# Kernel tuning notes

Hardware: AMD Instinct MI355X
Metric: run time of the kernel (lower is better)

Reference implementation:

```python
import jax, jax.numpy as jnp
import numpy as np

B, OUT, IN = 1024, 1024, 512


def setup_inputs() -> dict:
    key = jax.random.key(0)
    kx, kw = jax.random.split(key)
    X = jax.random.normal(kx, (B, IN), dtype=jnp.float32)
    # Xavier-uniform init for W [out_features, in_features]
    limit = float(np.sqrt(6.0 / (IN + OUT)))
    W = jax.random.uniform(kw, (OUT, IN), dtype=jnp.float32, minval=-limit, maxval=limit)
    return {"X": X, "W": W}


def reference(X, W):
    # tropical min-plus + max-plus 'matmul':
    # out[b,o] = min_i(W[o,i] + X[b,i]) + max_i(W[o,i] + X[b,i])
    S = X[:, None, :] + W[None, :, :]  # [B, OUT, IN]
    return jnp.min(S, axis=-1) + jnp.max(S, axis=-1)  # [B, OUT]
```

## Files before the change

### kernel.cpp

```cpp
#include <hip/hip_runtime.h>
#include <math.h>


typedef float f4 __attribute__((ext_vector_type(4)));

constexpr int B_DIM  = 1024;
constexpr int O_DIM  = 1024;
constexpr int IN_DIM = 512;

constexpr int NB = 64;
constexpr int NO = 16;
constexpr int KW = 64;

__global__ __launch_bounds__(512) void tropical_gemm(
    const float* __restrict__ X, const float* __restrict__ W,
    float* __restrict__ out) {
    __shared__ float lds[8192];

    const int tid  = threadIdx.x;
    const int w    = tid >> 6;
    const int lane = tid & 63;
    const int b0   = blockIdx.y * NB;
    const int o0   = blockIdx.x * NO;
    const int wu   = __builtin_amdgcn_readfirstlane(w);

    f4 xq[16];
    {
        const float* xp = X + (size_t)(b0 + lane) * IN_DIM + wu * KW;
#pragma unroll
        for (int j = 0; j < 16; ++j) xq[j] = *(const f4*)(xp + 4 * j);
    }

    const float* wbase = W + (size_t)o0 * IN_DIM + wu * KW;

    float mn[NO], mx[NO];
#pragma unroll
    for (int o = 0; o < NO; ++o) { mn[o] = INFINITY; mx[o] = -INFINITY; }

#pragma unroll
    for (int o = 0; o < NO; ++o) {
        const float* wr = wbase + (size_t)o * IN_DIM;
#pragma unroll
        for (int k = 0; k < KW; k += 2) {
            float s0 = xq[k >> 2][k & 3] + wr[k];
            float s1 = xq[(k + 1) >> 2][(k + 1) & 3] + wr[k + 1];
            asm("v_min3_f32 %0, %1, %2, %0"
                : "+v"(mn[o]) : "v"(s0), "v"(s1));
            asm("v_max3_f32 %0, %1, %2, %0"
                : "+v"(mx[o]) : "v"(s0), "v"(s1));
        }
    }

#define DUMP_STATE(slot)                                                      \
    do {                                                                      \
        float* p_ = lds + (slot) * 2048 + lane * 4;                           \
        _Pragma("unroll")                                                     \
        for (int c_ = 0; c_ < 4; ++c_) {                                      \
            f4 vn_ = {mn[4 * c_], mn[4 * c_ + 1], mn[4 * c_ + 2], mn[4 * c_ + 3]}; \
            f4 vx_ = {mx[4 * c_], mx[4 * c_ + 1], mx[4 * c_ + 2], mx[4 * c_ + 3]}; \
            *(f4*)(p_ + c_ * 256)       = vn_;                                \
            *(f4*)(p_ + (4 + c_) * 256) = vx_;                                \
        }                                                                     \
    } while (0)

#define MERGE_STATE(slot)                                                     \
    do {                                                                      \
        const float* p_ = lds + (slot) * 2048 + lane * 4;                     \
        _Pragma("unroll")                                                     \
        for (int c_ = 0; c_ < 4; ++c_) {                                      \
            f4 vn_ = *(const f4*)(p_ + c_ * 256);                             \
            f4 vx_ = *(const f4*)(p_ + (4 + c_) * 256);                       \
            mn[4 * c_]     = fminf(mn[4 * c_],     vn_[0]);                   \
            mn[4 * c_ + 1] = fminf(mn[4 * c_ + 1], vn_[1]);                   \
            mn[4 * c_ + 2] = fminf(mn[4 * c_ + 2], vn_[2]);                   \
            mn[4 * c_ + 3] = fminf(mn[4 * c_ + 3], vn_[3]);                   \
            mx[4 * c_]     = fmaxf(mx[4 * c_],     vx_[0]);                   \
            mx[4 * c_ + 1] = fmaxf(mx[4 * c_ + 1], vx_[1]);                   \
            mx[4 * c_ + 2] = fmaxf(mx[4 * c_ + 2], vx_[2]);                   \
            mx[4 * c_ + 3] = fmaxf(mx[4 * c_ + 3], vx_[3]);                   \
        }                                                                     \
    } while (0)

    __syncthreads();
    if (w >= 4) DUMP_STATE(w - 4);
    __syncthreads();
    if (w < 4) MERGE_STATE(w);
    __syncthreads();
    if (w == 2) DUMP_STATE(0);
    if (w == 3) DUMP_STATE(1);
    __syncthreads();
    if (w == 0) MERGE_STATE(0);
    if (w == 1) MERGE_STATE(1);
    __syncthreads();
    if (w == 1) DUMP_STATE(0);
    __syncthreads();
    if (w == 0) {
        MERGE_STATE(0);
        float* op = out + (size_t)(b0 + lane) * O_DIM + o0;
#pragma unroll
        for (int c = 0; c < 4; ++c) {
            f4 v = {mn[4 * c]     + mx[4 * c],
                    mn[4 * c + 1] + mx[4 * c + 1],
                    mn[4 * c + 2] + mx[4 * c + 2],
                    mn[4 * c + 3] + mx[4 * c + 3]};
            *(f4*)(op + 4 * c) = v;
        }
    }
#undef DUMP_STATE
#undef MERGE_STATE
}

extern "C" void kernel_launch(void* const* d_in, const int* in_sizes, int n_in,
                              void* d_out, int out_size, void* d_ws, size_t ws_size,
                              hipStream_t stream) {
    (void)in_sizes; (void)n_in; (void)d_ws; (void)ws_size; (void)out_size;
    const float* X = (const float*)d_in[0];
    const float* W = (const float*)d_in[1];
    float* out     = (float*)d_out;

    dim3 grid(O_DIM / NO, B_DIM / NB);
    tropical_gemm<<<grid, dim3(512), 0, stream>>>(X, W, out);
}
```

Baseline: 37.49 us.

## Stage W and X tiles through LDS with padded rows and software-pipelined W reads

The W tile for the block is copied into LDS once, and X rows are staged through a padded LDS buffer so each wave gets its 64-column slice via coalesced global loads instead of strided per-lane loads. The inner loop now reads W from LDS as f4 vectors, with four registers prefetched ahead of use, instead of issuing scalar global/constant loads per element. Launch bounds add a minimum occupancy hint. This trades extra LDS usage and eight barriers during X staging for fewer uncoalesced global accesses.

```diff
diff --git a/kernel.cpp b/kernel.cpp
--- a/kernel.cpp
+++ b/kernel.cpp
@@ -12,48 +12,99 @@
 constexpr int NO = 16;
 constexpr int KW = 64;
 
-__global__ __launch_bounds__(512) void tropical_gemm(
+constexpr int XREG     = 64 * 68;
+constexpr int WREG_OFF = XREG;
+
+__global__ __launch_bounds__(512, 4) void tropical_gemm(
     const float* __restrict__ X, const float* __restrict__ W,
     float* __restrict__ out) {
-    __shared__ float lds[8192];
+    __shared__ float lds[XREG + 16 * 512];
 
     const int tid  = threadIdx.x;
     const int w    = tid >> 6;
     const int lane = tid & 63;
     const int b0   = blockIdx.y * NB;
     const int o0   = blockIdx.x * NO;
-    const int wu   = __builtin_amdgcn_readfirstlane(w);
+
+    {
+        const int o   = tid >> 5;
+        const int kq0 = tid & 31;
+        const float* wp = W + (size_t)(o0 + o) * IN_DIM;
+        float* dst = lds + WREG_OFF + o * 512;
+#pragma unroll
+        for (int p = 0; p < 4; ++p) {
+            const int kq = kq0 + p * 32;
+            *(f4*)(dst + kq * 4) = *(const f4*)(wp + kq * 4);
+        }
+    }
 
     f4 xq[16];
     {
-        const float* xp = X + (size_t)(b0 + lane) * IN_DIM + wu * KW;
+        const int r  = tid >> 3;
+        const int q0 = tid & 7;
+        const float* xrow = X + (size_t)(b0 + r) * IN_DIM;
+        f4 ga = *(const f4*)(xrow + q0 * 4);
+        f4 gb = *(const f4*)(xrow + (q0 + 8) * 4);
+        for (int c = 0; c < 8; ++c) {
+            *(f4*)(lds + r * 68 + q0 * 4)       = ga;
+            *(f4*)(lds + r * 68 + (q0 + 8) * 4) = gb;
+            __syncthreads();
+            if (c < 7) {
+                ga = *(const f4*)(xrow + (c + 1) * 64 + q0 * 4);
+                gb = *(const f4*)(xrow + (c + 1) * 64 + (q0 + 8) * 4);
+            }
+            if (w == c) {
 #pragma unroll
-        for (int j = 0; j < 16; ++j) xq[j] = *(const f4*)(xp + 4 * j);
+                for (int j = 0; j < 16; ++j)
+                    xq[j] = *(const f4*)(lds + lane * 68 + j * 4);
+            }
+            __syncthreads();
+        }
     }
-
-    const float* wbase = W + (size_t)o0 * IN_DIM + wu * KW;
 
     float mn[NO], mx[NO];
 #pragma unroll
     for (int o = 0; o < NO; ++o) { mn[o] = INFINITY; mx[o] = -INFINITY; }
 
+    const char* wb = (const char*)(lds + WREG_OFF) + w * 256;
+
+#define LOADW(P, Q)                                                           \
+    P = *(const f4*)(wb + ((Q) >> 4) * 2048 + ((Q) & 15) * 16)
+
+#define CMPQ(P, Q)                                                            \
+    do {                                                                      \
+        float s0_ = xq[(Q) & 15][0] + P[0];                                   \
+        float s1_ = xq[(Q) & 15][1] + P[1];                                   \
+        float s2_ = xq[(Q) & 15][2] + P[2];                                   \
+        float s3_ = xq[(Q) & 15][3] + P[3];                                   \
+        asm("v_min3_f32 %0, %1, %2, %0"                                       \
+            : "+v"(mn[(Q) >> 4]) : "v"(s0_), "v"(s1_));                       \
+        asm("v_max3_f32 %0, %1, %2, %0"                                       \
+            : "+v"(mx[(Q) >> 4]) : "v"(s0_), "v"(s1_));                       \
+        asm("v_min3_f32 %0, %1, %2, %0"                                       \
+            : "+v"(mn[(Q) >> 4]) : "v"(s2_), "v"(s3_));                       \
+        asm("v_max3_f32 %0, %1, %2, %0"                                       \
+            : "+v"(mx[(Q) >> 4]) : "v"(s2_), "v"(s3_));                       \
+    } while (0)
+
+    {
+        f4 wA, wB, wC, wD;
+        LOADW(wA, 0); LOADW(wB, 1); LOADW(wC, 2); LOADW(wD, 3);
 #pragma unroll
-    for (int o = 0; o < NO; ++o) {
-        const float* wr = wbase + (size_t)o * IN_DIM;
-#pragma unroll
-        for (int k = 0; k < KW; k += 2) {
-            float s0 = xq[k >> 2][k & 3] + wr[k];
-            float s1 = xq[(k + 1) >> 2][(k + 1) & 3] + wr[k + 1];
-            asm("v_min3_f32 %0, %1, %2, %0"
-                : "+v"(mn[o]) : "v"(s0), "v"(s1));
-            asm("v_max3_f32 %0, %1, %2, %0"
-                : "+v"(mx[o]) : "v"(s0), "v"(s1));
+        for (int qp = 0; qp < 63; ++qp) {
+            CMPQ(wA, 4 * qp);     LOADW(wA, 4 * qp + 4);
+            CMPQ(wB, 4 * qp + 1); LOADW(wB, 4 * qp + 5);
+            CMPQ(wC, 4 * qp + 2); LOADW(wC, 4 * qp + 6);
+            CMPQ(wD, 4 * qp + 3); LOADW(wD, 4 * qp + 7);
         }
+        CMPQ(wA, 252); CMPQ(wB, 253); CMPQ(wC, 254); CMPQ(wD, 255);
     }
+#undef LOADW
+#undef CMPQ
 
 #define DUMP_STATE(slot)                                                      \
     do {                                                                      \
-        float* p_ = lds + (slot) * 2048 + lane * 4;                           \
+        float* p_ = lds + WREG_OFF + (slot) * 2048 + lane * 4;                \
         _Pragma("unroll")                                                     \
         for (int c_ = 0; c_ < 4; ++c_) {                                      \
             f4 vn_ = {mn[4 * c_], mn[4 * c_ + 1], mn[4 * c_ + 2], mn[4 * c_ + 3]}; \
@@ -65,7 +116,7 @@
 
 #define MERGE_STATE(slot)                                                     \
     do {                                                                      \
-        const float* p_ = lds + (slot) * 2048 + lane * 4;                     \
+        const float* p_ = lds + WREG_OFF + (slot) * 2048 + lane * 4;          \
         _Pragma("unroll")                                                     \
         for (int c_ = 0; c_ < 4; ++c_) {                                      \
             f4 vn_ = *(const f4*)(p_ + c_ * 256);                             \
```

After: 35.75 us. 4.6% less time.

## Use 64x64 register-tiled tropical GEMM with LDS staging and split-K combine

Applied to the files above, without the earlier changes.

Replaces the per-warp 64x16 layout, which re-read W rows from global memory, with a 64x64 output tile per block. Each lane now holds an 8x8 register micro-tile of min/max accumulators, and X/W are staged through double-buffered LDS. The K dimension is split across 4 waves plus optionally 2 blocks in z, with a separate combine kernel that reduces the partial min/max results from the workspace. This raises arithmetic intensity per load, at the cost of 128 accumulator registers, an extra kernel launch, and extra global traffic through the workspace.

```diff
diff --git a/kernel.cpp b/kernel.cpp
--- a/kernel.cpp
+++ b/kernel.cpp
@@ -3,88 +3,168 @@
 
 
 typedef float f4 __attribute__((ext_vector_type(4)));
+typedef float f2 __attribute__((ext_vector_type(2)));
 
 constexpr int B_DIM  = 1024;
 constexpr int O_DIM  = 1024;
 constexpr int IN_DIM = 512;
-
-constexpr int NB = 64;
-constexpr int NO = 16;
-constexpr int KW = 64;
-
-__global__ __launch_bounds__(512) void tropical_gemm(
+constexpr int TILE   = 64;
+constexpr int P      = B_DIM * O_DIM;
+
+template <int KSPLIT>
+__global__ __launch_bounds__(256) void tropical_gemm(
     const float* __restrict__ X, const float* __restrict__ W,
-    float* __restrict__ out) {
-    __shared__ float lds[8192];
+    float* __restrict__ out, float* __restrict__ ws) {
+    constexpr int KW     = (KSPLIT == 2) ? 64 : 128;
+    constexpr int NSTAGE = KW / 8;
+    __shared__ float lds[16384];
 
     const int tid  = threadIdx.x;
     const int w    = tid >> 6;
     const int lane = tid & 63;
-    const int b0   = blockIdx.y * NB;
-    const int o0   = blockIdx.x * NO;
-    const int wu   = __builtin_amdgcn_readfirstlane(w);
-
-    f4 xq[16];
-    {
-        const float* xp = X + (size_t)(b0 + lane) * IN_DIM + wu * KW;
-#pragma unroll
-        for (int j = 0; j < 16; ++j) xq[j] = *(const f4*)(xp + 4 * j);
+    const int im   = lane >> 3;
+    const int in_  = lane & 7;
+    const int b0   = blockIdx.y * TILE;
+    const int o0   = blockIdx.x * TILE;
+    const int kh   = (KSPLIT == 2) ? blockIdx.z : 0;
+    const int kbase = kh * (IN_DIM / KSPLIT) + w * KW;
+
+    const float* Xp = X + (size_t)(b0 + lane) * IN_DIM + kbase;
+    const float* Wp = W + (size_t)(o0 + lane) * IN_DIM + kbase;
+
+    float* wbase = &lds[w * 2048];
+    const int stw = ((lane & 7) >> 1) * 32 + (lane >> 3) * 4 + (lane & 1) * 2;
+
+    float mn[8][8], mx[8][8];
+#pragma unroll
+    for (int i = 0; i < 8; ++i)
+#pragma unroll
+        for (int j = 0; j < 8; ++j) { mn[i][j] = INFINITY; mx[i][j] = -INFINITY; }
+
+#define PF(S)                                                                 \
+    do {                                                                      \
+        xa = *(const f4*)(Xp + (S) * 8);                                      \
+        xb = *(const f4*)(Xp + (S) * 8 + 4);                                  \
+        wa = *(const f4*)(Wp + (S) * 8);                                      \
+        wb = *(const f4*)(Wp + (S) * 8 + 4);                                  \
+    } while (0)
+
+#define STAGE(BUF)                                                            \
+    do {                                                                      \
+        float* dX_ = wbase + (BUF) * 1024;                                    \
+        float* dW_ = dX_ + 512;                                               \
+        f2 x0_ = {xa[0], xa[1]}, x1_ = {xa[2], xa[3]};                        \
+        f2 x2_ = {xb[0], xb[1]}, x3_ = {xb[2], xb[3]};                        \
+        f2 w0_ = {wa[0], wa[1]}, w1_ = {wa[2], wa[3]};                        \
+        f2 w2_ = {wb[0], wb[1]}, w3_ = {wb[2], wb[3]};                        \
+        *(f2*)(dX_ + 0 * 128 + stw) = x0_;                                    \
+        *(f2*)(dX_ + 1 * 128 + stw) = x1_;                                    \
+        *(f2*)(dX_ + 2 * 128 + stw) = x2_;                                    \
+        *(f2*)(dX_ + 3 * 128 + stw) = x3_;                                    \
+        *(f2*)(dW_ + 0 * 128 + stw) = w0_;                                    \
+        *(f2*)(dW_ + 1 * 128 + stw) = w1_;                                    \
+        *(f2*)(dW_ + 2 * 128 + stw) = w2_;                                    \
+        *(f2*)(dW_ + 3 * 128 + stw) = w3_;                                    \
+    } while (0)
+
+#define KPBODY(KP, SX, SW)                                                    \
+    do {                                                                      \
+        f4 xq[4], wq[4];                                                      \
+        _Pragma("unroll")                                                     \
+        for (int q_ = 0; q_ < 4; ++q_)                                        \
+            xq[q_] = *(const f4*)((SX) + (KP) * 128 + q_ * 32 + im * 4);      \
+        _Pragma("unroll")                                                     \
+        for (int q_ = 0; q_ < 4; ++q_)                                        \
+            wq[q_] = *(const f4*)((SW) + (KP) * 128 + q_ * 32 + in_ * 4);     \
+        _Pragma("unroll")                                                     \
+        for (int q_ = 0; q_ < 4; ++q_) {                                      \
+            f2 xl_ = {xq[q_][0], xq[q_][1]};                                  \
+            f2 xh_ = {xq[q_][2], xq[q_][3]};                                  \
+            _Pragma("unroll")                                                 \
+            for (int p_ = 0; p_ < 4; ++p_) {                                  \
+                f2 wl_  = {wq[p_][0], wq[p_][1]};                             \
+                f2 wh_  = {wq[p_][2], wq[p_][3]};                             \
+                f2 s00_ = xl_ + wl_;                                          \
+                f2 s01_ = xl_ + wh_;                                          \
+                f2 s10_ = xh_ + wl_;                                          \
+                f2 s11_ = xh_ + wh_;                                          \
+                asm("v_min3_f32 %0, %1, %2, %0"                               \
+                    : "+v"(mn[2 * q_][2 * p_]) : "v"(s00_[0]), "v"(s00_[1])); \
+                asm("v_max3_f32 %0, %1, %2, %0"                               \
+                    : "+v"(mx[2 * q_][2 * p_]) : "v"(s00_[0]), "v"(s00_[1])); \
+                asm("v_min3_f32 %0, %1, %2, %0"                               \
+                    : "+v"(mn[2 * q_][2 * p_ + 1]) : "v"(s01_[0]), "v"(s01_[1])); \
+                asm("v_max3_f32 %0, %1, %2, %0"                               \
+                    : "+v"(mx[2 * q_][2 * p_ + 1]) : "v"(s01_[0]), "v"(s01_[1])); \
+                asm("v_min3_f32 %0, %1, %2, %0"                               \
+                    : "+v"(mn[2 * q_ + 1][2 * p_]) : "v"(s10_[0]), "v"(s10_[1])); \
+                asm("v_max3_f32 %0, %1, %2, %0"                               \
+                    : "+v"(mx[2 * q_ + 1][2 * p_]) : "v"(s10_[0]), "v"(s10_[1])); \
+                asm("v_min3_f32 %0, %1, %2, %0"                               \
+                    : "+v"(mn[2 * q_ + 1][2 * p_ + 1]) : "v"(s11_[0]), "v"(s11_[1])); \
+                asm("v_max3_f32 %0, %1, %2, %0"                               \
+                    : "+v"(mx[2 * q_ + 1][2 * p_ + 1]) : "v"(s11_[0]), "v"(s11_[1])); \
+            }                                                                 \
+        }                                                                     \
+    } while (0)
+
+    f4 xa, xb, wa, wb;
+    PF(0);
+    STAGE(0);
+    PF(1);
+
+#pragma unroll 1
+    for (int s = 0; s < NSTAGE; ++s) {
+        const float* sX = wbase + (s & 1) * 1024;
+        const float* sW = sX + 512;
+        KPBODY(0, sX, sW);
+        KPBODY(1, sX, sW);
+        if (s + 1 < NSTAGE) {
+            STAGE((s + 1) & 1);
+            if (s + 2 < NSTAGE) PF(s + 2);
+        }
+        KPBODY(2, sX, sW);
+        KPBODY(3, sX, sW);
     }
-
-    const float* wbase = W + (size_t)o0 * IN_DIM + wu * KW;
-
-    float mn[NO], mx[NO];
-#pragma unroll
-    for (int o = 0; o < NO; ++o) { mn[o] = INFINITY; mx[o] = -INFINITY; }
-
-#pragma unroll
-    for (int o = 0; o < NO; ++o) {
-        const float* wr = wbase + (size_t)o * IN_DIM;
-#pragma unroll
-        for (int k = 0; k < KW; k += 2) {
-            float s0 = xq[k >> 2][k & 3] + wr[k];
-            float s1 = xq[(k + 1) >> 2][(k + 1) & 3] + wr[k + 1];
-            asm("v_min3_f32 %0, %1, %2, %0"
-                : "+v"(mn[o]) : "v"(s0), "v"(s1));
-            asm("v_max3_f32 %0, %1, %2, %0"
-                : "+v"(mx[o]) : "v"(s0), "v"(s1));
-        }
-    }
-
-#define DUMP_STATE(slot)                                                      \
-    do {                                                                      \
-        float* p_ = lds + (slot) * 2048 + lane * 4;                           \
-        _Pragma("unroll")                                                     \
-        for (int c_ = 0; c_ < 4; ++c_) {                                      \
-            f4 vn_ = {mn[4 * c_], mn[4 * c_ + 1], mn[4 * c_ + 2], mn[4 * c_ + 3]}; \
-            f4 vx_ = {mx[4 * c_], mx[4 * c_ + 1], mx[4 * c_ + 2], mx[4 * c_ + 3]}; \
-            *(f4*)(p_ + c_ * 256)       = vn_;                                \
-            *(f4*)(p_ + (4 + c_) * 256) = vx_;                                \
+#undef PF
+#undef STAGE
+#undef KPBODY
+
+#define DUMP_STATE(SL)                                                        \
+    do {                                                                      \
+        float* p_ = lds + (SL) * 8192 + lane * 4;                             \
+        _Pragma("unroll")                                                     \
+        for (int r_ = 0; r_ < 8; ++r_) {                                      \
+            f4 a_ = {mn[r_][0], mn[r_][1], mn[r_][2], mn[r_][3]};             \
+            f4 b_ = {mn[r_][4], mn[r_][5], mn[r_][6], mn[r_][7]};             \
+            f4 c_ = {mx[r_][0], mx[r_][1], mx[r_][2], mx[r_][3]};             \
+            f4 d_ = {mx[r_][4], mx[r_][5], mx[r_][6], mx[r_][7]};             \
+            *(f4*)(p_ + (2 * r_) * 256)      = a_;                            \
+            *(f4*)(p_ + (2 * r_ + 1) * 256)  = b_;                            \
+            *(f4*)(p_ + (16 + 2 * r_) * 256) = c_;                            \
+            *(f4*)(p_ + (17 + 2 * r_) * 256) = d_;                            \
         }                                                                     \
     } while (0)
 
-#define MERGE_STATE(slot)                                                     \
-    do {                                                                      \
-        const float* p_ = lds + (slot) * 2048 + lane * 4;                     \
-        _Pragma("unroll")                                                     \
-        for (int c_ = 0; c_ < 4; ++c_) {                                      \
-            f4 vn_ = *(const f4*)(p_ + c_ * 256);                             \
-            f4 vx_ = *(const f4*)(p_ + (4 + c_) * 256);                       \
-            mn[4 * c_]     = fminf(mn[4 * c_],     vn_[0]);                   \
-            mn[4 * c_ + 1] = fminf(mn[4 * c_ + 1], vn_[1]);                   \
-            mn[4 * c_ + 2] = fminf(mn[4 * c_ + 2], vn_[2]);                   \
-            mn[4 * c_ + 3] = fminf(mn[4 * c_ + 3], vn_[3]);                   \
-            mx[4 * c_]     = fmaxf(mx[4 * c_],     vx_[0]);                   \
-            mx[4 * c_ + 1] = fmaxf(mx[4 * c_ + 1], vx_[1]);                   \
-            mx[4 * c_ + 2] = fmaxf(mx[4 * c_ + 2], vx_[2]);                   \
-            mx[4 * c_ + 3] = fmaxf(mx[4 * c_ + 3], vx_[3]);                   \
+#define MERGE_STATE(SL)                                                       \
+    do {                                                                      \
+        const float* p_ = lds + (SL) * 8192 + lane * 4;                       \
+        _Pragma("unroll")                                                     \
+        for (int r_ = 0; r_ < 8; ++r_) {                                      \
+            f4 a_ = *(const f4*)(p_ + (2 * r_) * 256);                        \
+            f4 b_ = *(const f4*)(p_ + (2 * r_ + 1) * 256);                    \
+            f4 c_ = *(const f4*)(p_ + (16 + 2 * r_) * 256);                   \
+            f4 d_ = *(const f4*)(p_ + (17 + 2 * r_) * 256);                   \
+            _Pragma("unroll")                                                 \
+            for (int j_ = 0; j_ < 4; ++j_) {                                  \
+                mn[r_][j_]     = fminf(mn[r_][j_],     a_[j_]);               \
+                mn[r_][4 + j_] = fminf(mn[r_][4 + j_], b_[j_]);               \
+                mx[r_][j_]     = fmaxf(mx[r_][j_],     c_[j_]);               \
+                mx[r_][4 + j_] = fmaxf(mx[r_][4 + j_], d_[j_]);               \
+            }                                                                 \
         }                                                                     \
     } while (0)
 
-    __syncthreads();
-    if (w >= 4) DUMP_STATE(w - 4);
-    __syncthreads();
-    if (w < 4) MERGE_STATE(w);
     __syncthreads();
     if (w == 2) DUMP_STATE(0);
     if (w == 3) DUMP_STATE(1);
@@ -96,28 +176,66 @@
     __syncthreads();
     if (w == 0) {
         MERGE_STATE(0);
-        float* op = out + (size_t)(b0 + lane) * O_DIM + o0;
-#pragma unroll
-        for (int c = 0; c < 4; ++c) {
-            f4 v = {mn[4 * c]     + mx[4 * c],
-                    mn[4 * c + 1] + mx[4 * c + 1],
-                    mn[4 * c + 2] + mx[4 * c + 2],
-                    mn[4 * c + 3] + mx[4 * c + 3]};
-            *(f4*)(op + 4 * c) = v;
+        if (KSPLIT == 2) {
+            float* mnp = ws + (size_t)kh * 2 * P;
+            float* mxp = mnp + P;
+#pragma unroll
+            for (int r = 0; r < 8; ++r) {
+                const size_t off = (size_t)(b0 + im * 8 + r) * O_DIM + o0 + in_ * 8;
+                f4 a = {mn[r][0], mn[r][1], mn[r][2], mn[r][3]};
+                f4 b = {mn[r][4], mn[r][5], mn[r][6], mn[r][7]};
+                f4 c = {mx[r][0], mx[r][1], mx[r][2], mx[r][3]};
+                f4 d = {mx[r][4], mx[r][5], mx[r][6], mx[r][7]};
+                *(f4*)(mnp + off)     = a;
+                *(f4*)(mnp + off + 4) = b;
+                *(f4*)(mxp + off)     = c;
+                *(f4*)(mxp + off + 4) = d;
+            }
+        } else {
+            float* op = out + (size_t)(b0 + im * 8) * O_DIM + o0 + in_ * 8;
+#pragma unroll
+            for (int r = 0; r < 8; ++r) {
+                f4 v0 = {mn[r][0] + mx[r][0], mn[r][1] + mx[r][1],
+                         mn[r][2] + mx[r][2], mn[r][3] + mx[r][3]};
+                f4 v1 = {mn[r][4] + mx[r][4], mn[r][5] + mx[r][5],
+                         mn[r][6] + mx[r][6], mn[r][7] + mx[r][7]};
+                *(f4*)(op + (size_t)r * O_DIM)     = v0;
+                *(f4*)(op + (size_t)r * O_DIM + 4) = v1;
+            }
         }
     }
 #undef DUMP_STATE
 #undef MERGE_STATE
 }
 
+__global__ __launch_bounds__(256) void combine_k(
+    const float* __restrict__ ws, float* __restrict__ out) {
+    const int i = (blockIdx.x * 256 + threadIdx.x) * 4;
+    f4 a = *(const f4*)(ws + i);
+    f4 b = *(const f4*)(ws + 2 * P + i);
+    f4 c = *(const f4*)(ws + P + i);
+    f4 d = *(const f4*)(ws + 3 * P + i);
+    f4 r;
+#pragma unroll
+    for (int j = 0; j < 4; ++j) r[j] = fminf(a[j], b[j]) + fmaxf(c[j], d[j]);
+    *(f4*)(out + i) = r;
+}
+
 extern "C" void kernel_launch(void* const* d_in, const int* in_sizes, int n_in,
                               void* d_out, int out_size, void* d_ws, size_t ws_size,
                               hipStream_t stream) {
-    (void)in_sizes; (void)n_in; (void)d_ws; (void)ws_size; (void)out_size;
+    (void)in_sizes; (void)n_in; (void)out_size;
     const float* X = (const float*)d_in[0];
     const float* W = (const float*)d_in[1];
     float* out     = (float*)d_out;
 
-    dim3 grid(O_DIM / NO, B_DIM / NB);
-    tropical_gemm<<<grid, dim3(512), 0, stream>>>(X, W, out);
+    const size_t need = (size_t)4 * P * sizeof(float);
+    if (ws_size >= need) {
+        tropical_gemm<2><<<dim3(16, 16, 2), dim3(256), 0, stream>>>(
+            X, W, out, (float*)d_ws);
+        combine_k<<<dim3(1024), dim3(256), 0, stream>>>((const float*)d_ws, out);
+    } else {
+        tropical_gemm<1><<<dim3(16, 16, 1), dim3(256), 0, stream>>>(
+            X, W, out, nullptr);
+    }
 }
```

New measurement: 46.45 us. 1.24x slower.
